# Kernel optimization log

Measured on AMD Instinct MI355X. Metric: run time of the kernel, lower is better.

Reference implementation:

```python
import jax, jax.numpy as jnp
import numpy as np
from functools import partial

POS_IOU_THRESHOLD = 0.5
NEG_IOU_THRESHOLD = 0.4
REG_LOSS_WEIGHT = 1.0
ALPHA, GAMMA = 0.25, 2.0
MIN_POS_TOPK = 10
NEG_POS_RATIO = 3

B, C, H, W, M = 16, 21, 256, 256, 20
N = H * W
IMG = 1024.0


def setup_inputs() -> dict:
    key = jax.random.key(0)
    k1, k2, k3, k4, k5 = jax.random.split(key, 5)
    cls_output = jax.random.normal(k1, (B, C, 1, H, W), dtype=jnp.float32)
    reg_output = 0.1 * jax.random.normal(k2, (B, 4, 1, H, W), dtype=jnp.float32)
    # dense grid anchors, stride 4, box size 32, xyxy
    ys, xs = jnp.meshgrid(jnp.arange(H, dtype=jnp.float32), jnp.arange(W, dtype=jnp.float32), indexing='ij')
    cx = (xs.reshape(-1) + 0.5) * (IMG / W)
    cy = (ys.reshape(-1) + 0.5) * (IMG / H)
    s = 16.0
    anchors = jnp.stack([cx - s, cy - s, cx + s, cy + s], axis=-1)  # [N,4]
    # random GT boxes inside the image
    ctr = jax.random.uniform(k3, (B, M, 2), minval=100.0, maxval=IMG - 100.0)
    wh = jax.random.uniform(k4, (B, M, 2), minval=20.0, maxval=200.0)
    target_boxes = jnp.concatenate([ctr - 0.5 * wh, ctr + 0.5 * wh], axis=-1).astype(jnp.float32)
    target_labels = 1 + jax.random.randint(k5, (B, M), 0, C - 1)
    neg_scores = jax.random.uniform(jax.random.fold_in(key, 7), (B, N), dtype=jnp.float32)
    return {"cls_output": cls_output, "reg_output": reg_output, "anchors": anchors,
            "target_boxes": target_boxes, "target_labels": target_labels, "neg_scores": neg_scores}


def _decode_boxes(reg, anchors):
    # standard (dx,dy,dw,dh) delta decode; anchors/pred in xyxy
    aw = anchors[:, 2] - anchors[:, 0]
    ah = anchors[:, 3] - anchors[:, 1]
    ax = anchors[:, 0] + 0.5 * aw
    ay = anchors[:, 1] + 0.5 * ah
    cx = ax + reg[:, 0] * aw
    cy = ay + reg[:, 1] * ah
    w = aw * jnp.exp(reg[:, 2])
    h = ah * jnp.exp(reg[:, 3])
    return jnp.stack([cx - 0.5 * w, cy - 0.5 * h, cx + 0.5 * w, cy + 0.5 * h], axis=-1)


def _pairwise_iou(a, b):
    # a: [N,4], b: [M,4] -> [N,M]
    area_a = (a[:, 2] - a[:, 0]) * (a[:, 3] - a[:, 1])
    area_b = (b[:, 2] - b[:, 0]) * (b[:, 3] - b[:, 1])
    lt = jnp.maximum(a[:, None, :2], b[None, :, :2])
    rb = jnp.minimum(a[:, None, 2:], b[None, :, 2:])
    wh = jnp.clip(rb - lt, 0.0)
    inter = wh[..., 0] * wh[..., 1]
    union = area_a[:, None] + area_b[None, :] - inter
    return inter / jnp.maximum(union, 1e-7)


def _giou_elementwise(a, b):
    # a,b: [P,4] -> [P]  (diag of generalized_box_iou)
    area_a = (a[:, 2] - a[:, 0]) * (a[:, 3] - a[:, 1])
    area_b = (b[:, 2] - b[:, 0]) * (b[:, 3] - b[:, 1])
    lt = jnp.maximum(a[:, :2], b[:, :2])
    rb = jnp.minimum(a[:, 2:], b[:, 2:])
    wh = jnp.clip(rb - lt, 0.0)
    inter = wh[:, 0] * wh[:, 1]
    union = area_a + area_b - inter
    iou = inter / jnp.maximum(union, 1e-7)
    elt = jnp.minimum(a[:, :2], b[:, :2])
    erb = jnp.maximum(a[:, 2:], b[:, 2:])
    ewh = jnp.clip(erb - elt, 0.0)
    enc = ewh[:, 0] * ewh[:, 1]
    return iou - (enc - union) / jnp.maximum(enc, 1e-7)


def _focal_from_ce(ce):
    p_t = jnp.exp(-ce)
    return ALPHA * (1.0 - p_t) ** GAMMA * ce


def _per_image(cls_i, reg_i, tb, tl, scores, anchors):
    # cls_i [N,C], reg_i [N,4], tb [M,4], tl [M], scores [N], anchors [N,4]
    n = cls_i.shape[0]
    decoded = _decode_boxes(reg_i, anchors)                 # [N,4]
    ious = _pairwise_iou(decoded, tb)                       # [N,M]
    max_ious = ious.max(axis=1)
    max_idx = ious.argmax(axis=1)
    pos_mask = max_ious >= POS_IOU_THRESHOLD
    neg_mask = max_ious < NEG_IOU_THRESHOLD
    # top-k fallback if too few positives
    _, top_idx = jax.lax.top_k(max_ious, MIN_POS_TOPK)
    fb_mask = jnp.zeros((n,), dtype=bool).at[top_idx].set(True)
    pos_mask = jnp.where(pos_mask.sum() < MIN_POS_TOPK, fb_mask, pos_mask)
    num_pos = pos_mask.sum()
    s = jnp.where(neg_mask, scores, jnp.inf)
    order = jnp.argsort(s)
    rank = jnp.zeros((n,), dtype=jnp.int32).at[order].set(jnp.arange(n, dtype=jnp.int32))
    sub_neg = neg_mask & (rank < NEG_POS_RATIO * num_pos)
    neg_mask = jnp.where(neg_mask.sum() > NEG_POS_RATIO * num_pos, sub_neg, neg_mask)
    total_samples = num_pos + neg_mask.sum()
    # focal classification loss
    logp = jax.nn.log_softmax(cls_i, axis=-1)               # [N,C]
    tgt_pos = tl[max_idx]                                   # [N]
    ce_pos = -jnp.take_along_axis(logp, tgt_pos[:, None], axis=1)[:, 0]
    ce_neg = -logp[:, 0]
    cls_loss_pos = jnp.sum(jnp.where(pos_mask, _focal_from_ce(ce_pos), 0.0))
    cls_loss_neg = jnp.sum(jnp.where(neg_mask, _focal_from_ce(ce_neg), 0.0))
    cls_loss = (cls_loss_pos + cls_loss_neg) / jnp.maximum(total_samples, 1)
    gt_matched = tb[max_idx]                                # [N,4]
    giou = _giou_elementwise(decoded, gt_matched)           # [N]
    reg_loss = jnp.sum(jnp.where(pos_mask, 1.0 - giou, 0.0)) / jnp.maximum(num_pos, 1)
    return cls_loss, reg_loss


def reference(cls_output, reg_output, anchors, target_boxes, target_labels, neg_scores):
    b, c = cls_output.shape[0], cls_output.shape[1]
    cls = cls_output.reshape(b, c, -1).transpose(0, 2, 1)   # [B,N,C]
    reg = reg_output.reshape(b, 4, -1).transpose(0, 2, 1)   # [B,N,4]
    cls_losses, reg_losses = jax.vmap(_per_image, in_axes=(0, 0, 0, 0, 0, None))(
        cls, reg, target_boxes, target_labels, neg_scores, anchors)
    total = cls_losses.mean() + REG_LOSS_WEIGHT * reg_losses.mean()
    return total
```

## Files before the change

kernel.cpp:

```cpp
#include <hip/hip_runtime.h>
#include <math.h>
#include <limits.h>

#define NB 16
#define NC 21
#define NANCH 65536
#define NM 20

#define POS_THR 0.5f
#define NEG_THR 0.4f
#define F_ALPHA 0.25f
#define MIN_POS_TOPK 10
#define NEG_POS_RATIO 3

#define QT 0.125f
#define ST 0.015625f
#define QCAP 4096
#define SCAP 4096
#define BCAP 512
#define APT 2
#define IOU_TPB 256

__global__ void k_zero(int* scal, float* sums) {
  int t = threadIdx.x;
  if (t < 6 * NB) scal[t] = 0;
  if (t < 3 * NB) sums[t] = 0.0f;
}

__global__ __launch_bounds__(IOU_TPB)
void k_iou(const float* __restrict__ reg, const float* __restrict__ anchors,
           const float* __restrict__ tb,
           float* __restrict__ miou, int* __restrict__ midx) {
  __shared__ float4 tbs4[NM];
  __shared__ float  tarea[NM];
  int b   = blockIdx.x >> 7;
  int blk = blockIdx.x & 127;
  int n0  = (blk << 9) + threadIdx.x;
  if (threadIdx.x < NM) {
    float4 t4 = ((const float4*)tb)[b * NM + threadIdx.x];
    tbs4[threadIdx.x] = t4;
    tarea[threadIdx.x] = (t4.z - t4.x) * (t4.w - t4.y);
  }
  __syncthreads();

  float dv[APT][4];
  float areaA[APT];
  #pragma unroll
  for (int j = 0; j < APT; ++j) {
    int n = n0 + j * IOU_TPB;
    float4 a4 = ((const float4*)anchors)[n];
    float aw = a4.z - a4.x, ah = a4.w - a4.y;
    float acx = a4.x + 0.5f * aw, acy = a4.y + 0.5f * ah;
    size_t rb = ((size_t)b * 4) * NANCH + n;
    float rx = reg[rb];
    float ry = reg[rb + (size_t)NANCH];
    float rw = reg[rb + 2 * (size_t)NANCH];
    float rh = reg[rb + 3 * (size_t)NANCH];
    float cx = acx + rx * aw, cy = acy + ry * ah;
    float w = aw * expf(rw), h = ah * expf(rh);
    dv[j][0] = cx - 0.5f * w;
    dv[j][1] = cy - 0.5f * h;
    dv[j][2] = cx + 0.5f * w;
    dv[j][3] = cy + 0.5f * h;
    areaA[j] = (dv[j][2] - dv[j][0]) * (dv[j][3] - dv[j][1]);
  }

  float bI[APT], bU[APT];
  int   bM[APT];
  {
    float4 t = tbs4[0];
    float ab = tarea[0];
    #pragma unroll
    for (int j = 0; j < APT; ++j) {
      float lx = fmaxf(dv[j][0], t.x), ly = fmaxf(dv[j][1], t.y);
      float rx2 = fminf(dv[j][2], t.z), ry2 = fminf(dv[j][3], t.w);
      float iw = fmaxf(rx2 - lx, 0.0f), ih = fmaxf(ry2 - ly, 0.0f);
      float inter = iw * ih;
      bI[j] = inter;
      bU[j] = areaA[j] + ab - inter;
      bM[j] = 0;
    }
  }
  #pragma unroll
  for (int m = 1; m < NM; ++m) {
    float4 t = tbs4[m];
    float ab = tarea[m];
    #pragma unroll
    for (int j = 0; j < APT; ++j) {
      float lx = fmaxf(dv[j][0], t.x), ly = fmaxf(dv[j][1], t.y);
      float rx2 = fminf(dv[j][2], t.z), ry2 = fminf(dv[j][3], t.w);
      float iw = fmaxf(rx2 - lx, 0.0f), ih = fmaxf(ry2 - ly, 0.0f);
      float inter = iw * ih;
      float uni = areaA[j] + ab - inter;
      if (inter * bU[j] > bI[j] * uni) { bI[j] = inter; bU[j] = uni; bM[j] = m; }
    }
  }

  #pragma unroll
  for (int j = 0; j < APT; ++j) {
    int n = n0 + j * IOU_TPB;
    size_t idx = (size_t)b * NANCH + n;
    miou[idx] = bI[j] / fmaxf(bU[j], 1e-7f);
    midx[idx] = bM[j];
  }
}

__device__ __forceinline__ void wave_append_lds(bool want, int lane,
                                                int* cnt, unsigned* kb, int* ki,
                                                unsigned bits, int n) {
  unsigned long long m = __ballot(want);
  if (!m) return;
  int leader = __ffsll((long long)m) - 1;
  int base = 0;
  if (lane == leader) base = atomicAdd(cnt, __popcll(m));
  base = __shfl(base, leader, 64);
  if (want) {
    int slot = base + __popcll(m & ((1ULL << lane) - 1ULL));
    kb[slot] = bits; ki[slot] = n;
  }
}

__global__ __launch_bounds__(1024)
void k_gather(const float* __restrict__ miou, const float* __restrict__ scores,
              int* __restrict__ pos_cnt, int* __restrict__ neg_cnt,
              unsigned* __restrict__ qcb, int* __restrict__ qci, int* __restrict__ qcnt,
              unsigned* __restrict__ scb, int* __restrict__ sci, int* __restrict__ scnt) {
  __shared__ unsigned lqB[1024];
  __shared__ int      lqI[1024];
  __shared__ unsigned lsB[1024];
  __shared__ int      lsI[1024];
  __shared__ int lqc, lsc, qbase, sbase;
  __shared__ int redp[16], redn[16];
  int b = blockIdx.x >> 6;
  int n = ((blockIdx.x & 63) << 10) | threadIdx.x;
  if (threadIdx.x == 0) { lqc = 0; lsc = 0; }
  __syncthreads();

  size_t idx = (size_t)b * NANCH + n;
  float q = miou[idx];
  float s = scores[idx];
  bool p  = (q >= POS_THR);
  bool ng = (q < NEG_THR);
  int lane = threadIdx.x & 63;
  int wid  = threadIdx.x >> 6;
  int cp = __popcll(__ballot(p));
  int cn = __popcll(__ballot(ng));
  if (lane == 0) { redp[wid] = cp; redn[wid] = cn; }

  wave_append_lds(q >= QT, lane, &lqc, lqB, lqI, __float_as_uint(q), n);
  wave_append_lds(ng && s < ST, lane, &lsc, lsB, lsI, __float_as_uint(s), n);
  __syncthreads();

  if (threadIdx.x == 0) {
    int tp = 0, tn = 0;
    for (int w = 0; w < 16; ++w) { tp += redp[w]; tn += redn[w]; }
    if (tp) atomicAdd(&pos_cnt[b], tp);
    if (tn) atomicAdd(&neg_cnt[b], tn);
    qbase = lqc ? atomicAdd(&qcnt[b], lqc) : 0;
    sbase = lsc ? atomicAdd(&scnt[b], lsc) : 0;
  }
  __syncthreads();

  for (int j = threadIdx.x; j < lqc; j += 1024) {
    int slot = qbase + j;
    if (slot < QCAP) {
      qcb[(size_t)b * QCAP + slot] = lqB[j];
      qci[(size_t)b * QCAP + slot] = lqI[j];
    }
  }
  for (int j = threadIdx.x; j < lsc; j += 1024) {
    int slot = sbase + j;
    if (slot < SCAP) {
      scb[(size_t)b * SCAP + slot] = lsB[j];
      sci[(size_t)b * SCAP + slot] = lsI[j];
    }
  }
}

__global__ __launch_bounds__(1024)
void k_sel(const unsigned* __restrict__ qcb, const int* __restrict__ qci,
           const int* __restrict__ qcnt,
           const unsigned* __restrict__ scb, const int* __restrict__ sci,
           const int* __restrict__ scnt,
           const int* __restrict__ pos_cnt, const int* __restrict__ neg_cnt,
           int* __restrict__ num_pos, int* __restrict__ use_fb,
           int* __restrict__ subsample, int* __restrict__ total_samples,
           int* __restrict__ top10,
           unsigned* __restrict__ vbits_out, int* __restrict__ idx_cut,
           int* __restrict__ flagq, int* __restrict__ flags) {
  if (blockIdx.x < NB) {
    __shared__ unsigned cB[QCAP];
    __shared__ int      cI[QCAP];
    __shared__ unsigned wv[16];
    __shared__ int      wi[16], wsl[16];
    __shared__ int      sel[MIN_POS_TOPK];
    int b = blockIdx.x;
    int pc = pos_cnt[b], nc = neg_cnt[b];
    int fb = (pc < MIN_POS_TOPK) ? 1 : 0;
    int np = fb ? MIN_POS_TOPK : pc;
    int k = NEG_POS_RATIO * np;
    int sub = (nc > k) ? 1 : 0;
    if (threadIdx.x == 0) {
      num_pos[b] = np; use_fb[b] = fb; subsample[b] = sub;
      total_samples[b] = sub ? (np + k) : (np + nc);
    }
    if (!fb) return;
    int E = qcnt[b];
    if (E < MIN_POS_TOPK || E > QCAP) {
      if (threadIdx.x == 0) flagq[b] = 1;
      return;
    }
    for (int j = threadIdx.x; j < E; j += 1024) {
      cB[j] = qcb[(size_t)b * QCAP + j];
      cI[j] = qci[(size_t)b * QCAP + j];
    }
    __syncthreads();
    int lane = threadIdx.x & 63;
    int wid  = threadIdx.x >> 6;
    for (int it = 0; it < MIN_POS_TOPK; ++it) {
      unsigned bb = 0u; int bi = INT_MAX, bs = -1;
      for (int j = threadIdx.x; j < E; j += 1024) {
        unsigned v = cB[j];
        if (v > bb || (v == bb && cI[j] < bi)) { bb = v; bi = cI[j]; bs = j; }
      }
      #pragma unroll
      for (int m = 32; m >= 1; m >>= 1) {
        unsigned ov = __shfl_xor(bb, m, 64);
        int oi = __shfl_xor(bi, m, 64);
        int os = __shfl_xor(bs, m, 64);
        if (ov > bb || (ov == bb && oi < bi)) { bb = ov; bi = oi; bs = os; }
      }
      if (lane == 0) { wv[wid] = bb; wi[wid] = bi; wsl[wid] = bs; }
      __syncthreads();
      if (threadIdx.x == 0) {
        unsigned eb = 0u; int ei = INT_MAX, es = -1;
        for (int w = 0; w < 16; ++w) {
          if (wv[w] > eb || (wv[w] == eb && wi[w] < ei)) { eb = wv[w]; ei = wi[w]; es = wsl[w]; }
        }
        sel[it] = ei;
        cB[es] = 0u;
      }
      __syncthreads();
    }
    if (threadIdx.x < MIN_POS_TOPK) top10[b * MIN_POS_TOPK + threadIdx.x] = sel[threadIdx.x];
  } else {
    __shared__ unsigned hist[256];
    __shared__ unsigned bbB[BCAP];
    __shared__ int      bbI[BCAP];
    __shared__ int s_bkt, s_below, s_cnt;
    int b = blockIdx.x - NB;
    int pc = pos_cnt[b], nc = neg_cnt[b];
    int np = (pc < MIN_POS_TOPK) ? MIN_POS_TOPK : pc;
    int k = NEG_POS_RATIO * np;
    if (nc <= k) {
      if (threadIdx.x == 0) { vbits_out[b] = 0u; idx_cut[b] = -1; }
      return;
    }
    int E = scnt[b];
    if (E < k || E > SCAP) {
      if (threadIdx.x == 0) flags[b] = 1;
      return;
    }
    if (threadIdx.x < 256) hist[threadIdx.x] = 0u;
    if (threadIdx.x == 0) s_cnt = 0;
    __syncthreads();
    for (int j = threadIdx.x; j < E; j += 1024) {
      float s = __uint_as_float(scb[(size_t)b * SCAP + j]);
      unsigned bin = (unsigned)(s * 16384.0f);
      atomicAdd(&hist[bin > 255u ? 255u : bin], 1u);
    }
    __syncthreads();
    if (threadIdx.x == 0) {
      unsigned cum = 0; int bkt = 255;
      for (int t = 0; t < 256; ++t) {
        if (cum + hist[t] >= (unsigned)k) { bkt = t; break; }
        cum += hist[t];
      }
      s_bkt = bkt; s_below = (int)cum;
    }
    __syncthreads();
    int bkt = s_bkt;
    for (int j = threadIdx.x; j < E; j += 1024) {
      unsigned sb = scb[(size_t)b * SCAP + j];
      float s = __uint_as_float(sb);
      unsigned bin = (unsigned)(s * 16384.0f);
      if ((int)(bin > 255u ? 255u : bin) == bkt) {
        int slot = atomicAdd(&s_cnt, 1);
        if (slot < BCAP) { bbB[slot] = sb; bbI[slot] = sci[(size_t)b * SCAP + j]; }
      }
    }
    __syncthreads();
    int cnt = s_cnt;
    int r = k - s_below;
    if (cnt > BCAP || r < 1 || r > cnt) {
      if (threadIdx.x == 0) flags[b] = 1;
      return;
    }
    for (int e = threadIdx.x; e < cnt; e += 1024) {
      unsigned mb = bbB[e]; int mi_ = bbI[e];
      int rank = 0;
      for (int j = 0; j < cnt; ++j) {
        unsigned ob = bbB[j]; int oi = bbI[j];
        rank += (ob < mb || (ob == mb && oi < mi_)) ? 1 : 0;
      }
      if (rank == r - 1) { vbits_out[b] = mb; idx_cut[b] = mi_; }
    }
  }
}

__device__ __forceinline__ void bitonic_sort(unsigned long long* key, int S) {
  for (int kk = 2; kk <= S; kk <<= 1) {
    for (int jj = kk >> 1; jj > 0; jj >>= 1) {
      for (int i = threadIdx.x; i < S; i += 1024) {
        int ixj = i ^ jj;
        if (ixj > i) {
          bool up = ((i & kk) == 0);
          unsigned long long a = key[i], c = key[ixj];
          if ((a > c) == up) { key[i] = c; key[ixj] = a; }
        }
      }
      __syncthreads();
    }
  }
}

__global__ __launch_bounds__(1024)
void k_rescue(const float* __restrict__ miou, const float* __restrict__ scores,
              const int* __restrict__ flagq, const int* __restrict__ flags,
              const int* __restrict__ num_pos,
              int* __restrict__ top10,
              unsigned* __restrict__ vbits_out, int* __restrict__ idx_cut) {
  int b = blockIdx.x;
  int fq = flagq[b], fs = flags[b];
  if (!fq && !fs) return;
  const float* mi = miou + (size_t)b * NANCH;
  const float* sc = scores + (size_t)b * NANCH;
  int lane = threadIdx.x & 63;
  int wid  = threadIdx.x >> 6;

  __shared__ unsigned long long buf64[4096];
  __shared__ unsigned qh[64];
  __shared__ int s_thr, s_cnt, s_ok;

  if (fq) {
    if (threadIdx.x < 64) qh[threadIdx.x] = 0u;
    if (threadIdx.x == 0) { s_cnt = 0; s_ok = 0; }
    __syncthreads();
    for (int n = threadIdx.x; n < NANCH; n += 1024) {
      float q = mi[n];
      if (q >= QT) {
        unsigned bin = (unsigned)(q * 64.0f);
        if (bin > 63u) bin = 63u;
        atomicAdd(&qh[bin], 1u);
      }
    }
    __syncthreads();
    if (threadIdx.x == 0) {
      unsigned cum = 0; int t = -1;
      for (int i = 63; i >= 8; --i) {
        cum += qh[i];
        if (cum >= (unsigned)MIN_POS_TOPK) { t = i; break; }
      }
      if (t < 0) t = 8;
      unsigned c = 0;
      for (int i = t; i < 64; ++i) c += qh[i];
      s_thr = t; s_cnt = 0;
      s_ok = (c >= (unsigned)MIN_POS_TOPK && c <= 4096u) ? 1 : 0;
    }
    __syncthreads();
    if (s_ok) {
      int t = s_thr;
      for (int n = threadIdx.x; n < NANCH; n += 1024) {
        float q = mi[n];
        if (q >= QT) {
          unsigned bin = (unsigned)(q * 64.0f);
          if (bin > 63u) bin = 63u;
          if ((int)bin >= t) {
            int slot = atomicAdd(&s_cnt, 1);
            if (slot < 4096)
              buf64[slot] = ((unsigned long long)(~__float_as_uint(q)) << 32) | (unsigned)n;
          }
        }
      }
      __syncthreads();
      int E = s_cnt < 4096 ? s_cnt : 4096;
      int S = 16; while (S < E) S <<= 1;
      for (int j = threadIdx.x; j < S; j += 1024)
        if (j >= E) buf64[j] = 0xFFFFFFFFFFFFFFFFULL;
      __syncthreads();
      bitonic_sort(buf64, S);
      if (threadIdx.x < MIN_POS_TOPK)
        top10[b * MIN_POS_TOPK + threadIdx.x] = (int)(unsigned)(buf64[threadIdx.x] & 0xFFFFFFFFu);
    } else {
      __shared__ float fsv[16];
      __shared__ int   fsi[16];
      __shared__ int   fsel[MIN_POS_TOPK];
      for (int it = 0; it < MIN_POS_TOPK; ++it) {
        float bv = -1.0f; int bi = NANCH;
        for (int n = threadIdx.x; n < NANCH; n += 1024) {
          bool skip = false;
          for (int s2 = 0; s2 < it; ++s2) if (fsel[s2] == n) skip = true;
          if (skip) continue;
          float v = mi[n];
          if (v > bv || (v == bv && n < bi)) { bv = v; bi = n; }
        }
        #pragma unroll
        for (int m = 32; m >= 1; m >>= 1) {
          float ov = __shfl_xor(bv, m, 64);
          int   oi = __shfl_xor(bi, m, 64);
          if (ov > bv || (ov == bv && oi < bi)) { bv = ov; bi = oi; }
        }
        if (lane == 0) { fsv[wid] = bv; fsi[wid] = bi; }
        __syncthreads();
        if (threadIdx.x == 0) {
          float bb = -1.0f; int bj = NANCH;
          for (int w = 0; w < 16; ++w)
            if (fsv[w] > bb || (fsv[w] == bb && fsi[w] < bj)) { bb = fsv[w]; bj = fsi[w]; }
          fsel[it] = bj;
        }
        __syncthreads();
      }
      if (threadIdx.x < MIN_POS_TOPK) top10[b * MIN_POS_TOPK + threadIdx.x] = fsel[threadIdx.x];
    }
    __syncthreads();
  }

  if (fs) {
    __shared__ unsigned lsh[256];
    __shared__ int s_bkt, s_below, s_cnt2;
    int k = NEG_POS_RATIO * num_pos[b];
    if (threadIdx.x < 256) lsh[threadIdx.x] = 0u;
    if (threadIdx.x == 0) s_cnt2 = 0;
    __syncthreads();
    for (int n = threadIdx.x; n < NANCH; n += 1024) {
      if (mi[n] < NEG_THR) {
        unsigned bin = (unsigned)(sc[n] * 256.0f);
        if (bin > 255u) bin = 255u;
        atomicAdd(&lsh[bin], 1u);
      }
    }
    __syncthreads();
    if (threadIdx.x == 0) {
      unsigned cum = 0; int bkt = 255;
      for (int t = 0; t < 256; ++t) {
        if (cum + lsh[t] >= (unsigned)k) { bkt = t; break; }
        cum += lsh[t];
      }
      s_bkt = bkt; s_below = (int)cum;
    }
    __syncthreads();
    int bkt = s_bkt;
    for (int n = threadIdx.x; n < NANCH; n += 1024) {
      if (mi[n] < NEG_THR) {
        float s = sc[n];
        unsigned bin = (unsigned)(s * 256.0f);
        if (bin > 255u) bin = 255u;
        if ((int)bin == bkt) {
          int slot = atomicAdd(&s_cnt2, 1);
          if (slot < 4096)
            buf64[slot] = ((unsigned long long)__float_as_uint(s) << 32) | (unsigned)n;
        }
      }
    }
    __syncthreads();
    int E = s_cnt2 < 4096 ? s_cnt2 : 4096;
    int S = 16; while (S < E) S <<= 1;
    for (int j = threadIdx.x; j < S; j += 1024)
      if (j >= E) buf64[j] = 0xFFFFFFFFFFFFFFFFULL;
    __syncthreads();
    bitonic_sort(buf64, S);
    int r = k - s_below;
    if (threadIdx.x == 0 && r >= 1 && r <= E) {
      unsigned long long kv = buf64[r - 1];
      vbits_out[b] = (unsigned)(kv >> 32);
      idx_cut[b]  = (int)(unsigned)(kv & 0xFFFFFFFFu);
    }
  }
}

__global__ __launch_bounds__(256)
void k_loss(const float* __restrict__ cls, const float* __restrict__ reg,
            const float* __restrict__ anchors, const float* __restrict__ tb,
            const int* __restrict__ tl, const float* __restrict__ scores,
            const float* __restrict__ miou, const int* __restrict__ midx,
            const int* __restrict__ use_fb, const int* __restrict__ top10,
            const int* __restrict__ subsample, const unsigned* __restrict__ vbits,
            const int* __restrict__ idx_cut,
            float* __restrict__ sums ) {
  int b = blockIdx.x >> 8;
  int n = ((blockIdx.x & 255) << 8) | threadIdx.x;
  __shared__ int s_top10[MIN_POS_TOPK];
  __shared__ int s_usefb, s_sub, s_cut;
  __shared__ unsigned s_vb;
  __shared__ float accp, accn, accr;
  if (threadIdx.x < MIN_POS_TOPK) s_top10[threadIdx.x] = top10[b * MIN_POS_TOPK + threadIdx.x];
  if (threadIdx.x == 0) {
    s_usefb = use_fb[b]; s_sub = subsample[b]; s_cut = idx_cut[b]; s_vb = vbits[b];
    accp = 0.0f; accn = 0.0f; accr = 0.0f;
  }
  __syncthreads();

  size_t idx = (size_t)b * NANCH + n;
  float mi = miou[idx];

  bool pos;
  if (s_usefb) {
    pos = false;
    #pragma unroll
    for (int i = 0; i < MIN_POS_TOPK; ++i) pos |= (s_top10[i] == n);
  } else {
    pos = (mi >= POS_THR);
  }
  bool neg = (mi < NEG_THR);
  bool nsel = false;
  if (neg) {
    if (!s_sub) nsel = true;
    else {
      unsigned sb = __float_as_uint(scores[idx]);
      nsel = (sb < s_vb) || (sb == s_vb && n <= s_cut);
    }
  }

  float cp = 0.0f, cn = 0.0f, rg = 0.0f;
  if (pos || nsel) {
    int mx = 0, t = 0;
    if (pos) { mx = midx[idx]; t = tl[b * NM + mx]; }
    size_t cb = ((size_t)b * NC) * NANCH + n;
    float mxl = -3.0e38f, l0 = 0.0f, lt = 0.0f;
    for (int c = 0; c < NC; ++c) {
      float l = cls[cb + (size_t)c * NANCH];
      if (c == 0) l0 = l;
      if (c == t) lt = l;
      mxl = fmaxf(mxl, l);
    }
    float se = 0.0f;
    for (int c = 0; c < NC; ++c) {
      float l = cls[cb + (size_t)c * NANCH];
      se += expf(l - mxl);
    }
    float lse = mxl + logf(se);
    if (nsel) {
      float ce = lse - l0;
      float pt = expf(-ce);
      float om = 1.0f - pt;
      cn = F_ALPHA * om * om * ce;
    }
    if (pos) {
      float ce = lse - lt;
      float pt = expf(-ce);
      float om = 1.0f - pt;
      cp = F_ALPHA * om * om * ce;
      const float4 a4 = ((const float4*)anchors)[n];
      float aw = a4.z - a4.x, ah = a4.w - a4.y;
      float acx = a4.x + 0.5f * aw, acy = a4.y + 0.5f * ah;
      size_t rb = ((size_t)b * 4) * NANCH + n;
      float rx = reg[rb];
      float ry = reg[rb + (size_t)NANCH];
      float rw = reg[rb + 2 * (size_t)NANCH];
      float rh = reg[rb + 3 * (size_t)NANCH];
      float ccx = acx + rx * aw, ccy = acy + ry * ah;
      float w = aw * expf(rw), h = ah * expf(rh);
      float d0 = ccx - 0.5f * w, d1 = ccy - 0.5f * h;
      float d2 = ccx + 0.5f * w, d3 = ccy + 0.5f * h;
      const float* g = tb + ((size_t)b * NM + mx) * 4;
      float gx1 = g[0], gy1 = g[1], gx2 = g[2], gy2 = g[3];
      float area_a = (d2 - d0) * (d3 - d1);
      float area_b = (gx2 - gx1) * (gy2 - gy1);
      float lx = fmaxf(d0, gx1), ly = fmaxf(d1, gy1);
      float rx2 = fminf(d2, gx2), ry2 = fminf(d3, gy2);
      float iw = fmaxf(rx2 - lx, 0.0f), ih = fmaxf(ry2 - ly, 0.0f);
      float inter = iw * ih;
      float uni = area_a + area_b - inter;
      float iou = inter / fmaxf(uni, 1e-7f);
      float ex1 = fminf(d0, gx1), ey1 = fminf(d1, gy1);
      float ex2 = fmaxf(d2, gx2), ey2 = fmaxf(d3, gy2);
      float ew = fmaxf(ex2 - ex1, 0.0f), eh = fmaxf(ey2 - ey1, 0.0f);
      float enc = ew * eh;
      float giou = iou - (enc - uni) / fmaxf(enc, 1e-7f);
      rg = 1.0f - giou;
    }
  }

  if (cp != 0.0f) atomicAdd(&accp, cp);
  if (cn != 0.0f) atomicAdd(&accn, cn);
  if (rg != 0.0f) atomicAdd(&accr, rg);
  __syncthreads();
  if (threadIdx.x == 0) {
    if (accp != 0.0f) atomicAdd(&sums[b * 3 + 0], accp);
    if (accn != 0.0f) atomicAdd(&sums[b * 3 + 1], accn);
    if (accr != 0.0f) atomicAdd(&sums[b * 3 + 2], accr);
  }
}

__global__ void k_final(const float* __restrict__ sums,
                        const int* __restrict__ total_samples,
                        const int* __restrict__ num_pos,
                        float* __restrict__ out) {
  int t = threadIdx.x;
  float cm = 0.0f, rm = 0.0f;
  if (t < NB) {
    int ts = total_samples[t]; if (ts < 1) ts = 1;
    int np = num_pos[t]; if (np < 1) np = 1;
    cm = (sums[t * 3 + 0] + sums[t * 3 + 1]) / (float)ts;
    rm = sums[t * 3 + 2] / (float)np;
  }
  #pragma unroll
  for (int m = 8; m >= 1; m >>= 1) {
    cm += __shfl_down(cm, m, 64);
    rm += __shfl_down(rm, m, 64);
  }
  if (t == 0) out[0] = cm / (float)NB + rm / (float)NB;
}

extern "C" void kernel_launch(void* const* d_in, const int* in_sizes, int n_in,
                              void* d_out, int out_size, void* d_ws, size_t ws_size,
                              hipStream_t stream) {
  const float* cls     = (const float*)d_in[0];
  const float* reg     = (const float*)d_in[1];
  const float* anchors = (const float*)d_in[2];
  const float* tb      = (const float*)d_in[3];
  const int*   tl      = (const int*)d_in[4];
  const float* scores  = (const float*)d_in[5];
  float* out = (float*)d_out;

  char* ws = (char*)d_ws;
  size_t off = 0;
  float* miou = (float*)(ws + off);            off += (size_t)4 * NB * NANCH;
  int*   midx = (int*)(ws + off);              off += (size_t)4 * NB * NANCH;
  unsigned* qcb = (unsigned*)(ws + off);       off += (size_t)4 * NB * QCAP;
  int*   qci = (int*)(ws + off);               off += (size_t)4 * NB * QCAP;
  unsigned* scb = (unsigned*)(ws + off);       off += (size_t)4 * NB * SCAP;
  int*   sci = (int*)(ws + off);               off += (size_t)4 * NB * SCAP;
  int* scal = (int*)(ws + off);
  int* pos_cnt  = scal;
  int* neg_cnt  = scal + NB;
  int* qcnt     = scal + 2 * NB;
  int* scnt     = scal + 3 * NB;
  int* flagq    = scal + 4 * NB;
  int* flags    = scal + 5 * NB;
  int* num_pos       = scal + 6 * NB;
  int* use_fb        = scal + 7 * NB;
  int* subsample     = scal + 8 * NB;
  int* idx_cut       = scal + 9 * NB;
  unsigned* vbits    = (unsigned*)(scal + 10 * NB);
  int* total_samples = scal + 11 * NB;
  int* top10         = scal + 12 * NB;
  float* sums        = (float*)(scal + 12 * NB + MIN_POS_TOPK * NB);

  k_zero<<<1, 256, 0, stream>>>(scal, sums);
  k_iou<<<NB * 128, IOU_TPB, 0, stream>>>(reg, anchors, tb, miou, midx);
  k_gather<<<NB * 64, 1024, 0, stream>>>(miou, scores, pos_cnt, neg_cnt,
                                         qcb, qci, qcnt, scb, sci, scnt);
  k_sel<<<2 * NB, 1024, 0, stream>>>(qcb, qci, qcnt, scb, sci, scnt,
                                     pos_cnt, neg_cnt,
                                     num_pos, use_fb, subsample, total_samples,
                                     top10, vbits, idx_cut, flagq, flags);
  k_rescue<<<NB, 1024, 0, stream>>>(miou, scores, flagq, flags, num_pos,
                                    top10, vbits, idx_cut);
  k_loss<<<NB * 256, 256, 0, stream>>>(cls, reg, anchors, tb, tl, scores,
                                       miou, midx, use_fb, top10, subsample,
                                       vbits, idx_cut, sums);
  k_final<<<1, 64, 0, stream>>>(sums, total_samples, num_pos, out);
}
```

Before: 84.57 us.

## Fold zeroing, rescue, and final reduction into neighboring kernels to cut launches

Removes three kernel launches. Workspace zeroing moves into block 0 of the IoU kernel, the fallback rescue paths move inline into the selection kernel (replacing bitonic sort with argmax/rank selection), and the final reduction runs in the last-finishing loss block via an atomic done counter. This removes per-launch overhead and the serial dependency chain, at the cost of a larger shared-memory footprint in the selection kernel and a last-block-done pattern that depends on correct fences. BCAP is also raised to accommodate the fallback path.

```diff
diff --git a/kernel.cpp b/kernel.cpp
--- a/kernel.cpp
+++ b/kernel.cpp
@@ -17,20 +17,20 @@
 #define ST 0.015625f
 #define QCAP 4096
 #define SCAP 4096
-#define BCAP 512
+#define BCAP 2048
 #define APT 2
 #define IOU_TPB 256
-
-__global__ void k_zero(int* scal, float* sums) {
-  int t = threadIdx.x;
-  if (t < 6 * NB) scal[t] = 0;
-  if (t < 3 * NB) sums[t] = 0.0f;
-}
 
 __global__ __launch_bounds__(IOU_TPB)
 void k_iou(const float* __restrict__ reg, const float* __restrict__ anchors,
            const float* __restrict__ tb,
-           float* __restrict__ miou, int* __restrict__ midx) {
+           float* __restrict__ miou, int* __restrict__ midx,
+           int* __restrict__ zints, float* __restrict__ zsums) {
+  if (blockIdx.x == 0) {
+    int t = threadIdx.x;
+    if (t < 4 * NB + 1) zints[t] = 0;
+    if (t < 3 * NB) zsums[t] = 0.0f;
+  }
   __shared__ float4 tbs4[NM];
   __shared__ float  tarea[NM];
   int b   = blockIdx.x >> 7;
@@ -177,23 +177,55 @@
   }
 }
 
+__device__ __forceinline__ void argmax10(unsigned* cB, int* cI, int E,
+                                         int* top10_out) {
+  __shared__ unsigned wv[16];
+  __shared__ int      wi_[16], wsl[16];
+  __shared__ int      sel[MIN_POS_TOPK];
+  int lane = threadIdx.x & 63;
+  int wid  = threadIdx.x >> 6;
+  for (int it = 0; it < MIN_POS_TOPK; ++it) {
+    unsigned bb = 0u; int bi = INT_MAX, bs = -1;
+    for (int j = threadIdx.x; j < E; j += 1024) {
+      unsigned v = cB[j];
+      if (v > bb || (v == bb && cI[j] < bi)) { bb = v; bi = cI[j]; bs = j; }
+    }
+    #pragma unroll
+    for (int m = 32; m >= 1; m >>= 1) {
+      unsigned ov = __shfl_xor(bb, m, 64);
+      int oi = __shfl_xor(bi, m, 64);
+      int os = __shfl_xor(bs, m, 64);
+      if (ov > bb || (ov == bb && oi < bi)) { bb = ov; bi = oi; bs = os; }
+    }
+    if (lane == 0) { wv[wid] = bb; wi_[wid] = bi; wsl[wid] = bs; }
+    __syncthreads();
+    if (threadIdx.x == 0) {
+      unsigned eb = 0u; int ei = INT_MAX, es = -1;
+      for (int w = 0; w < 16; ++w) {
+        if (wv[w] > eb || (wv[w] == eb && wi_[w] < ei)) { eb = wv[w]; ei = wi_[w]; es = wsl[w]; }
+      }
+      sel[it] = ei;
+      cB[es] = 0u;
+    }
+    __syncthreads();
+  }
+  if (threadIdx.x < MIN_POS_TOPK) top10_out[threadIdx.x] = sel[threadIdx.x];
+}
+
 __global__ __launch_bounds__(1024)
 void k_sel(const unsigned* __restrict__ qcb, const int* __restrict__ qci,
            const int* __restrict__ qcnt,
            const unsigned* __restrict__ scb, const int* __restrict__ sci,
            const int* __restrict__ scnt,
            const int* __restrict__ pos_cnt, const int* __restrict__ neg_cnt,
+           const float* __restrict__ miou, const float* __restrict__ scores,
            int* __restrict__ num_pos, int* __restrict__ use_fb,
            int* __restrict__ subsample, int* __restrict__ total_samples,
            int* __restrict__ top10,
-           unsigned* __restrict__ vbits_out, int* __restrict__ idx_cut,
-           int* __restrict__ flagq, int* __restrict__ flags) {
+           unsigned* __restrict__ vbits_out, int* __restrict__ idx_cut) {
+  __shared__ unsigned cB[QCAP];
+  __shared__ int      cI[QCAP];
   if (blockIdx.x < NB) {
-    __shared__ unsigned cB[QCAP];
-    __shared__ int      cI[QCAP];
-    __shared__ unsigned wv[16];
-    __shared__ int      wi[16], wsl[16];
-    __shared__ int      sel[MIN_POS_TOPK];
     int b = blockIdx.x;
     int pc = pos_cnt[b], nc = neg_cnt[b];
     int fb = (pc < MIN_POS_TOPK) ? 1 : 0;
@@ -206,143 +238,18 @@
     }
     if (!fb) return;
     int E = qcnt[b];
-    if (E < MIN_POS_TOPK || E > QCAP) {
-      if (threadIdx.x == 0) flagq[b] = 1;
+    if (E >= MIN_POS_TOPK && E <= QCAP) {
+      for (int j = threadIdx.x; j < E; j += 1024) {
+        cB[j] = qcb[(size_t)b * QCAP + j];
+        cI[j] = qci[(size_t)b * QCAP + j];
+      }
+      __syncthreads();
+      argmax10(cB, cI, E, top10 + b * MIN_POS_TOPK);
       return;
     }
-    for (int j = threadIdx.x; j < E; j += 1024) {
-      cB[j] = qcb[(size_t)b * QCAP + j];
-      cI[j] = qci[(size_t)b * QCAP + j];
-    }
-    __syncthreads();
-    int lane = threadIdx.x & 63;
-    int wid  = threadIdx.x >> 6;
-    for (int it = 0; it < MIN_POS_TOPK; ++it) {
-      unsigned bb = 0u; int bi = INT_MAX, bs = -1;
-      for (int j = threadIdx.x; j < E; j += 1024) {
-        unsigned v = cB[j];
-        if (v > bb || (v == bb && cI[j] < bi)) { bb = v; bi = cI[j]; bs = j; }
-      }
-      #pragma unroll
-      for (int m = 32; m >= 1; m >>= 1) {
-        unsigned ov = __shfl_xor(bb, m, 64);
-        int oi = __shfl_xor(bi, m, 64);
-        int os = __shfl_xor(bs, m, 64);
-        if (ov > bb || (ov == bb && oi < bi)) { bb = ov; bi = oi; bs = os; }
-      }
-      if (lane == 0) { wv[wid] = bb; wi[wid] = bi; wsl[wid] = bs; }
-      __syncthreads();
-      if (threadIdx.x == 0) {
-        unsigned eb = 0u; int ei = INT_MAX, es = -1;
-        for (int w = 0; w < 16; ++w) {
-          if (wv[w] > eb || (wv[w] == eb && wi[w] < ei)) { eb = wv[w]; ei = wi[w]; es = wsl[w]; }
-        }
-        sel[it] = ei;
-        cB[es] = 0u;
-      }
-      __syncthreads();
-    }
-    if (threadIdx.x < MIN_POS_TOPK) top10[b * MIN_POS_TOPK + threadIdx.x] = sel[threadIdx.x];
-  } else {
-    __shared__ unsigned hist[256];
-    __shared__ unsigned bbB[BCAP];
-    __shared__ int      bbI[BCAP];
-    __shared__ int s_bkt, s_below, s_cnt;
-    int b = blockIdx.x - NB;
-    int pc = pos_cnt[b], nc = neg_cnt[b];
-    int np = (pc < MIN_POS_TOPK) ? MIN_POS_TOPK : pc;
-    int k = NEG_POS_RATIO * np;
-    if (nc <= k) {
-      if (threadIdx.x == 0) { vbits_out[b] = 0u; idx_cut[b] = -1; }
-      return;
-    }
-    int E = scnt[b];
-    if (E < k || E > SCAP) {
-      if (threadIdx.x == 0) flags[b] = 1;
-      return;
-    }
-    if (threadIdx.x < 256) hist[threadIdx.x] = 0u;
-    if (threadIdx.x == 0) s_cnt = 0;
-    __syncthreads();
-    for (int j = threadIdx.x; j < E; j += 1024) {
-      float s = __uint_as_float(scb[(size_t)b * SCAP + j]);
-      unsigned bin = (unsigned)(s * 16384.0f);
-      atomicAdd(&hist[bin > 255u ? 255u : bin], 1u);
-    }
-    __syncthreads();
-    if (threadIdx.x == 0) {
-      unsigned cum = 0; int bkt = 255;
-      for (int t = 0; t < 256; ++t) {
-        if (cum + hist[t] >= (unsigned)k) { bkt = t; break; }
-        cum += hist[t];
-      }
-      s_bkt = bkt; s_below = (int)cum;
-    }
-    __syncthreads();
-    int bkt = s_bkt;
-    for (int j = threadIdx.x; j < E; j += 1024) {
-      unsigned sb = scb[(size_t)b * SCAP + j];
-      float s = __uint_as_float(sb);
-      unsigned bin = (unsigned)(s * 16384.0f);
-      if ((int)(bin > 255u ? 255u : bin) == bkt) {
-        int slot = atomicAdd(&s_cnt, 1);
-        if (slot < BCAP) { bbB[slot] = sb; bbI[slot] = sci[(size_t)b * SCAP + j]; }
-      }
-    }
-    __syncthreads();
-    int cnt = s_cnt;
-    int r = k - s_below;
-    if (cnt > BCAP || r < 1 || r > cnt) {
-      if (threadIdx.x == 0) flags[b] = 1;
-      return;
-    }
-    for (int e = threadIdx.x; e < cnt; e += 1024) {
-      unsigned mb = bbB[e]; int mi_ = bbI[e];
-      int rank = 0;
-      for (int j = 0; j < cnt; ++j) {
-        unsigned ob = bbB[j]; int oi = bbI[j];
-        rank += (ob < mb || (ob == mb && oi < mi_)) ? 1 : 0;
-      }
-      if (rank == r - 1) { vbits_out[b] = mb; idx_cut[b] = mi_; }
-    }
-  }
-}
-
-__device__ __forceinline__ void bitonic_sort(unsigned long long* key, int S) {
-  for (int kk = 2; kk <= S; kk <<= 1) {
-    for (int jj = kk >> 1; jj > 0; jj >>= 1) {
-      for (int i = threadIdx.x; i < S; i += 1024) {
-        int ixj = i ^ jj;
-        if (ixj > i) {
-          bool up = ((i & kk) == 0);
-          unsigned long long a = key[i], c = key[ixj];
-          if ((a > c) == up) { key[i] = c; key[ixj] = a; }
-        }
-      }
-      __syncthreads();
-    }
-  }
-}
-
-__global__ __launch_bounds__(1024)
-void k_rescue(const float* __restrict__ miou, const float* __restrict__ scores,
-              const int* __restrict__ flagq, const int* __restrict__ flags,
-              const int* __restrict__ num_pos,
-              int* __restrict__ top10,
-              unsigned* __restrict__ vbits_out, int* __restrict__ idx_cut) {
-  int b = blockIdx.x;
-  int fq = flagq[b], fs = flags[b];
-  if (!fq && !fs) return;
-  const float* mi = miou + (size_t)b * NANCH;
-  const float* sc = scores + (size_t)b * NANCH;
-  int lane = threadIdx.x & 63;
-  int wid  = threadIdx.x >> 6;
-
-  __shared__ unsigned long long buf64[4096];
-  __shared__ unsigned qh[64];
-  __shared__ int s_thr, s_cnt, s_ok;
-
-  if (fq) {
+    const float* mi = miou + (size_t)b * NANCH;
+    __shared__ unsigned qh[64];
+    __shared__ int s_thr, s_cnt, s_ok;
     if (threadIdx.x < 64) qh[threadIdx.x] = 0u;
     if (threadIdx.x == 0) { s_cnt = 0; s_ok = 0; }
     __syncthreads();
@@ -364,8 +271,8 @@
       if (t < 0) t = 8;
       unsigned c = 0;
       for (int i = t; i < 64; ++i) c += qh[i];
-      s_thr = t; s_cnt = 0;
-      s_ok = (c >= (unsigned)MIN_POS_TOPK && c <= 4096u) ? 1 : 0;
+      s_thr = t;
+      s_ok = (c >= (unsigned)MIN_POS_TOPK && c <= (unsigned)QCAP) ? 1 : 0;
     }
     __syncthreads();
     if (s_ok) {
@@ -377,24 +284,22 @@
           if (bin > 63u) bin = 63u;
           if ((int)bin >= t) {
             int slot = atomicAdd(&s_cnt, 1);
-            if (slot < 4096)
-              buf64[slot] = ((unsigned long long)(~__float_as_uint(q)) << 32) | (unsigned)n;
+            if (slot < QCAP) {
+              cB[slot] = __float_as_uint(q);
+              cI[slot] = n;
+            }
           }
         }
       }
       __syncthreads();
-      int E = s_cnt < 4096 ? s_cnt : 4096;
-      int S = 16; while (S < E) S <<= 1;
-      for (int j = threadIdx.x; j < S; j += 1024)
-        if (j >= E) buf64[j] = 0xFFFFFFFFFFFFFFFFULL;
-      __syncthreads();
-      bitonic_sort(buf64, S);
-      if (threadIdx.x < MIN_POS_TOPK)
-        top10[b * MIN_POS_TOPK + threadIdx.x] = (int)(unsigned)(buf64[threadIdx.x] & 0xFFFFFFFFu);
+      int E2 = s_cnt < QCAP ? s_cnt : QCAP;
+      argmax10(cB, cI, E2, top10 + b * MIN_POS_TOPK);
     } else {
       __shared__ float fsv[16];
       __shared__ int   fsi[16];
       __shared__ int   fsel[MIN_POS_TOPK];
+      int lane = threadIdx.x & 63;
+      int wid  = threadIdx.x >> 6;
       for (int it = 0; it < MIN_POS_TOPK; ++it) {
         float bv = -1.0f; int bi = NANCH;
         for (int n = threadIdx.x; n < NANCH; n += 1024) {
@@ -422,29 +327,89 @@
       }
       if (threadIdx.x < MIN_POS_TOPK) top10[b * MIN_POS_TOPK + threadIdx.x] = fsel[threadIdx.x];
     }
-    __syncthreads();
-  }
-
-  if (fs) {
-    __shared__ unsigned lsh[256];
-    __shared__ int s_bkt, s_below, s_cnt2;
-    int k = NEG_POS_RATIO * num_pos[b];
-    if (threadIdx.x < 256) lsh[threadIdx.x] = 0u;
-    if (threadIdx.x == 0) s_cnt2 = 0;
+  } else {
+    __shared__ unsigned hist[256];
+    __shared__ unsigned* bbB;
+    __shared__ int s_bkt, s_below, s_cnt, s_fail;
+    unsigned* BB = cB;
+    int*      BI = cI;
+    int b = blockIdx.x - NB;
+    int pc = pos_cnt[b], nc = neg_cnt[b];
+    int np = (pc < MIN_POS_TOPK) ? MIN_POS_TOPK : pc;
+    int k = NEG_POS_RATIO * np;
+    if (nc <= k) {
+      if (threadIdx.x == 0) { vbits_out[b] = 0u; idx_cut[b] = -1; }
+      return;
+    }
+    int E = scnt[b];
+    bool cand_ok = (E >= k && E <= SCAP);
+    if (threadIdx.x == 0) s_fail = 0;
+    if (cand_ok) {
+      if (threadIdx.x < 256) hist[threadIdx.x] = 0u;
+      if (threadIdx.x == 0) s_cnt = 0;
+      __syncthreads();
+      for (int j = threadIdx.x; j < E; j += 1024) {
+        float s = __uint_as_float(scb[(size_t)b * SCAP + j]);
+        unsigned bin = (unsigned)(s * 16384.0f);
+        atomicAdd(&hist[bin > 255u ? 255u : bin], 1u);
+      }
+      __syncthreads();
+      if (threadIdx.x == 0) {
+        unsigned cum = 0; int bkt = 255;
+        for (int t = 0; t < 256; ++t) {
+          if (cum + hist[t] >= (unsigned)k) { bkt = t; break; }
+          cum += hist[t];
+        }
+        s_bkt = bkt; s_below = (int)cum;
+      }
+      __syncthreads();
+      int bkt = s_bkt;
+      for (int j = threadIdx.x; j < E; j += 1024) {
+        unsigned sb = scb[(size_t)b * SCAP + j];
+        float s = __uint_as_float(sb);
+        unsigned bin = (unsigned)(s * 16384.0f);
+        if ((int)(bin > 255u ? 255u : bin) == bkt) {
+          int slot = atomicAdd(&s_cnt, 1);
+          if (slot < BCAP) { BB[slot] = sb; BI[slot] = sci[(size_t)b * SCAP + j]; }
+        }
+      }
+      __syncthreads();
+      int cnt = s_cnt;
+      int r = k - s_below;
+      if (cnt > BCAP || r < 1 || r > cnt) {
+        if (threadIdx.x == 0) s_fail = 1;
+      } else {
+        for (int e = threadIdx.x; e < cnt; e += 1024) {
+          unsigned mb = BB[e]; int mi_ = BI[e];
+          int rank = 0;
+          for (int j = 0; j < cnt; ++j) {
+            unsigned ob = BB[j]; int oi = BI[j];
+            rank += (ob < mb || (ob == mb && oi < mi_)) ? 1 : 0;
+          }
+          if (rank == r - 1) { vbits_out[b] = mb; idx_cut[b] = mi_; }
+        }
+      }
+      __syncthreads();
+      if (!s_fail) return;
+    }
+    const float* mi = miou + (size_t)b * NANCH;
+    const float* sc = scores + (size_t)b * NANCH;
+    if (threadIdx.x < 256) hist[threadIdx.x] = 0u;
+    if (threadIdx.x == 0) s_cnt = 0;
     __syncthreads();
     for (int n = threadIdx.x; n < NANCH; n += 1024) {
       if (mi[n] < NEG_THR) {
         unsigned bin = (unsigned)(sc[n] * 256.0f);
         if (bin > 255u) bin = 255u;
-        atomicAdd(&lsh[bin], 1u);
+        atomicAdd(&hist[bin], 1u);
       }
     }
     __syncthreads();
     if (threadIdx.x == 0) {
       unsigned cum = 0; int bkt = 255;
       for (int t = 0; t < 256; ++t) {
-        if (cum + lsh[t] >= (unsigned)k) { bkt = t; break; }
-        cum += lsh[t];
+        if (cum + hist[t] >= (unsigned)k) { bkt = t; break; }
+        cum += hist[t];
       }
       s_bkt = bkt; s_below = (int)cum;
     }
@@ -456,24 +421,28 @@
         unsigned bin = (unsigned)(s * 256.0f);
         if (bin > 255u) bin = 255u;
         if ((int)bin == bkt) {
-          int slot = atomicAdd(&s_cnt2, 1);
-          if (slot < 4096)
-            buf64[slot] = ((unsigned long long)__float_as_uint(s) << 32) | (unsigned)n;
-        }
-      }
-    }
-    __syncthreads();
-    int E = s_cnt2 < 4096 ? s_cnt2 : 4096;
-    int S = 16; while (S < E) S <<= 1;
-    for (int j = threadIdx.x; j < S; j += 1024)
-      if (j >= E) buf64[j] = 0xFFFFFFFFFFFFFFFFULL;
-    __syncthreads();
-    bitonic_sort(buf64, S);
+          int slot = atomicAdd(&s_cnt, 1);
+          if (slot < BCAP) {
+            BB[slot] = __float_as_uint(s);
+            BI[slot] = n;
+          }
+        }
+      }
+    }
+    __syncthreads();
+    int cnt = s_cnt < BCAP ? s_cnt : BCAP;
     int r = k - s_below;
-    if (threadIdx.x == 0 && r >= 1 && r <= E) {
-      unsigned long long kv = buf64[r - 1];
-      vbits_out[b] = (unsigned)(kv >> 32);
-      idx_cut[b]  = (int)(unsigned)(kv & 0xFFFFFFFFu);
+    if (threadIdx.x == 0 && (r < 1 || r > cnt)) {
+      vbits_out[b] = 0xFFFFFFFFu; idx_cut[b] = NANCH;
+    }
+    for (int e = threadIdx.x; e < cnt; e += 1024) {
+      unsigned mb = BB[e]; int mi_ = BI[e];
+      int rank = 0;
+      for (int j = 0; j < cnt; ++j) {
+        unsigned ob = BB[j]; int oi = BI[j];
+        rank += (ob < mb || (ob == mb && oi < mi_)) ? 1 : 0;
+      }
+      if (rank == r - 1) { vbits_out[b] = mb; idx_cut[b] = mi_; }
     }
   }
 }
@@ -486,13 +455,16 @@
             const int* __restrict__ use_fb, const int* __restrict__ top10,
             const int* __restrict__ subsample, const unsigned* __restrict__ vbits,
             const int* __restrict__ idx_cut,
-            float* __restrict__ sums ) {
+            float* __restrict__ sums ,
+            const int* __restrict__ total_samples, const int* __restrict__ num_pos,
+            int* __restrict__ done_cnt, float* __restrict__ out) {
   int b = blockIdx.x >> 8;
   int n = ((blockIdx.x & 255) << 8) | threadIdx.x;
   __shared__ int s_top10[MIN_POS_TOPK];
   __shared__ int s_usefb, s_sub, s_cut;
   __shared__ unsigned s_vb;
   __shared__ float accp, accn, accr;
+  __shared__ int s_last;
   if (threadIdx.x < MIN_POS_TOPK) s_top10[threadIdx.x] = top10[b * MIN_POS_TOPK + threadIdx.x];
   if (threadIdx.x == 0) {
     s_usefb = use_fb[b]; s_sub = subsample[b]; s_cut = idx_cut[b]; s_vb = vbits[b];
@@ -589,27 +561,33 @@
     if (accp != 0.0f) atomicAdd(&sums[b * 3 + 0], accp);
     if (accn != 0.0f) atomicAdd(&sums[b * 3 + 1], accn);
     if (accr != 0.0f) atomicAdd(&sums[b * 3 + 2], accr);
-  }
-}
-
-__global__ void k_final(const float* __restrict__ sums,
-                        const int* __restrict__ total_samples,
-                        const int* __restrict__ num_pos,
-                        float* __restrict__ out) {
-  int t = threadIdx.x;
-  float cm = 0.0f, rm = 0.0f;
-  if (t < NB) {
-    int ts = total_samples[t]; if (ts < 1) ts = 1;
-    int np = num_pos[t]; if (np < 1) np = 1;
-    cm = (sums[t * 3 + 0] + sums[t * 3 + 1]) / (float)ts;
-    rm = sums[t * 3 + 2] / (float)np;
-  }
-  #pragma unroll
-  for (int m = 8; m >= 1; m >>= 1) {
-    cm += __shfl_down(cm, m, 64);
-    rm += __shfl_down(rm, m, 64);
-  }
-  if (t == 0) out[0] = cm / (float)NB + rm / (float)NB;
+    __threadfence();
+    int done = atomicAdd(done_cnt, 1);
+    s_last = (done == (int)gridDim.x - 1) ? 1 : 0;
+  }
+  __syncthreads();
+
+  if (s_last) {
+    int t = threadIdx.x;
+    if (t < 64) {
+      float cm = 0.0f, rm = 0.0f;
+      if (t < NB) {
+        int ts = total_samples[t]; if (ts < 1) ts = 1;
+        int np = num_pos[t]; if (np < 1) np = 1;
+        float s0 = atomicAdd(&sums[t * 3 + 0], 0.0f);
+        float s1 = atomicAdd(&sums[t * 3 + 1], 0.0f);
+        float s2 = atomicAdd(&sums[t * 3 + 2], 0.0f);
+        cm = (s0 + s1) / (float)ts;
+        rm = s2 / (float)np;
+      }
+      #pragma unroll
+      for (int m = 8; m >= 1; m >>= 1) {
+        cm += __shfl_down(cm, m, 64);
+        rm += __shfl_down(rm, m, 64);
+      }
+      if (t == 0) out[0] = cm / (float)NB + rm / (float)NB;
+    }
+  }
 }
 
 extern "C" void kernel_launch(void* const* d_in, const int* in_sizes, int n_in,
@@ -636,29 +614,26 @@
   int* neg_cnt  = scal + NB;
   int* qcnt     = scal + 2 * NB;
   int* scnt     = scal + 3 * NB;
-  int* flagq    = scal + 4 * NB;
-  int* flags    = scal + 5 * NB;
-  int* num_pos       = scal + 6 * NB;
-  int* use_fb        = scal + 7 * NB;
-  int* subsample     = scal + 8 * NB;
-  int* idx_cut       = scal + 9 * NB;
-  unsigned* vbits    = (unsigned*)(scal + 10 * NB);
-  int* total_samples = scal + 11 * NB;
-  int* top10         = scal + 12 * NB;
-  float* sums        = (float*)(scal + 12 * NB + MIN_POS_TOPK * NB);
-
-  k_zero<<<1, 256, 0, stream>>>(scal, sums);
-  k_iou<<<NB * 128, IOU_TPB, 0, stream>>>(reg, anchors, tb, miou, midx);
+  int* done_cnt = scal + 4 * NB;
+  int* num_pos       = scal + 4 * NB + 1;
+  int* use_fb        = scal + 5 * NB + 1;
+  int* subsample     = scal + 6 * NB + 1;
+  int* idx_cut       = scal + 7 * NB + 1;
+  unsigned* vbits    = (unsigned*)(scal + 8 * NB + 1);
+  int* total_samples = scal + 9 * NB + 1;
+  int* top10         = scal + 10 * NB + 1;
+  float* sums        = (float*)(scal + 10 * NB + 1 + MIN_POS_TOPK * NB);
+
+  k_iou<<<NB * 128, IOU_TPB, 0, stream>>>(reg, anchors, tb, miou, midx,
+                                          scal, sums);
   k_gather<<<NB * 64, 1024, 0, stream>>>(miou, scores, pos_cnt, neg_cnt,
                                          qcb, qci, qcnt, scb, sci, scnt);
   k_sel<<<2 * NB, 1024, 0, stream>>>(qcb, qci, qcnt, scb, sci, scnt,
-                                     pos_cnt, neg_cnt,
+                                     pos_cnt, neg_cnt, miou, scores,
                                      num_pos, use_fb, subsample, total_samples,
-                                     top10, vbits, idx_cut, flagq, flags);
-  k_rescue<<<NB, 1024, 0, stream>>>(miou, scores, flagq, flags, num_pos,
-                                    top10, vbits, idx_cut);
+                                     top10, vbits, idx_cut);
   k_loss<<<NB * 256, 256, 0, stream>>>(cls, reg, anchors, tb, tl, scores,
                                        miou, midx, use_fb, top10, subsample,
-                                       vbits, idx_cut, sums);
-  k_final<<<1, 64, 0, stream>>>(sums, total_samples, num_pos, out);
+                                       vbits, idx_cut, sums,
+                                       total_samples, num_pos, done_cnt, out);
 }
```

Result: slower. 147.5 us (+74.5%).
